# Optimization experiments

Hardware: AMD Instinct MI355X
Metric: run time of the kernel (lower is better)

The kernel has to match this reference:

```python
import jax, jax.numpy as jnp
import numpy as np

N_HEAD = 12
N_EMBD = 768


def setup_inputs() -> dict:
    key = jax.random.key(0)
    ks = jax.random.split(key, 5)
    B, T, C = 8, 1024, N_EMBD
    x = jax.random.normal(ks[0], (B, T, C), dtype=jnp.float32)
    # c_attn: Linear(C, 3C); c_proj: Linear(C, C). PyTorch Linear: y = x @ W.T + b
    s = 1.0 / np.sqrt(C)
    W_attn = jax.random.uniform(ks[1], (3 * C, C), minval=-s, maxval=s, dtype=jnp.float32)
    b_attn = jax.random.uniform(ks[2], (3 * C,), minval=-s, maxval=s, dtype=jnp.float32)
    W_proj = jax.random.uniform(ks[3], (C, C), minval=-s, maxval=s, dtype=jnp.float32)
    b_proj = jax.random.uniform(ks[4], (C,), minval=-s, maxval=s, dtype=jnp.float32)
    return {"x": x, "W_attn": W_attn, "b_attn": b_attn, "W_proj": W_proj, "b_proj": b_proj}


def reference(x, W_attn, b_attn, W_proj, b_proj):
    B, T, C = x.shape
    H = N_HEAD
    hs = C // H  # head size
    qkv = x @ W_attn.T + b_attn  # [B, T, 3C]
    q, k, v = jnp.split(qkv, 3, axis=2)
    # [B, T, H, hs] -> [B, H, T, hs]
    q = q.reshape(B, T, H, hs).transpose(0, 2, 1, 3)
    k = k.reshape(B, T, H, hs).transpose(0, 2, 1, 3)
    v = v.reshape(B, T, H, hs).transpose(0, 2, 1, 3)
    att = jnp.einsum('bhqd,bhkd->bhqk', q, k) * (1.0 / np.sqrt(hs))
    causal = jnp.tril(jnp.ones((T, T), dtype=bool))
    att = jnp.where(causal, att, -jnp.inf)
    att = jax.nn.softmax(att, axis=-1)
    y = jnp.einsum('bhqk,bhkd->bhqd', att, v)  # [B, H, T, hs]
    y = y.transpose(0, 2, 1, 3).reshape(B, T, C)
    return y @ W_proj.T + b_proj
```

## Files before the change

### kernel.cpp

```cpp
#include <hip/hip_runtime.h>

typedef unsigned short u16;
typedef __attribute__((ext_vector_type(8))) __bf16 bf16x8;
typedef __attribute__((ext_vector_type(4))) float f32x4;
typedef __attribute__((ext_vector_type(4))) int i32x4;

#define MFMA16(a, b, c) __builtin_amdgcn_mfma_f32_16x16x32_bf16(a, b, c, 0, 0, 0)

__device__ __forceinline__ u16 f2b(float f) {
  __bf16 h = (__bf16)f;
  return __builtin_bit_cast(u16, h);
}

__device__ __forceinline__ void gl_lds16(const void* g, void* l) {
  __builtin_amdgcn_global_load_lds(
      (const __attribute__((address_space(1))) void*)g,
      (__attribute__((address_space(3))) void*)l, 16, 0, 0);
}

__device__ __forceinline__ bf16x8 ldf(const void* p) {
  return __builtin_bit_cast(bf16x8, *(const i32x4*)p);
}

__global__ __launch_bounds__(256) void cvt3_kernel(
    const float4* __restrict__ a, ushort4* __restrict__ oa, int na4,
    const float4* __restrict__ b, ushort4* __restrict__ ob, int nb4,
    const float4* __restrict__ c, ushort4* __restrict__ oc, int nc4) {
  const int step = gridDim.x * blockDim.x;
  const int t0 = blockIdx.x * blockDim.x + threadIdx.x;
  for (int i = t0; i < na4; i += step) {
    float4 v = a[i];
    ushort4 o; o.x = f2b(v.x); o.y = f2b(v.y); o.z = f2b(v.z); o.w = f2b(v.w);
    oa[i] = o;
  }
  for (int i = t0; i < nb4; i += step) {
    float4 v = b[i];
    ushort4 o; o.x = f2b(v.x); o.y = f2b(v.y); o.z = f2b(v.z); o.w = f2b(v.w);
    ob[i] = o;
  }
  for (int i = t0; i < nc4; i += step) {
    float4 v = c[i];
    ushort4 o; o.x = f2b(v.x); o.y = f2b(v.y); o.z = f2b(v.z); o.w = f2b(v.w);
    oc[i] = o;
  }
}

template <int BM, int EPI>
__global__ __launch_bounds__(256, 3) void gemm4(
    const u16* __restrict__ A, const u16* __restrict__ B,
    const float* __restrict__ bias, int M, int N, int K,
    u16* __restrict__ q_s, u16* __restrict__ k_s, u16* __restrict__ vt_s,
    float* __restrict__ outf) {
  constexpr int BN = 192;
  constexpr int MR = BM / 32;
  constexpr int NR = 6;
  constexpr int IA = BM / 32;
  constexpr int IB = 6;
  __shared__ __align__(16) u16 As[BM * 64];
  __shared__ __align__(16) u16 Bs[BN * 64];
  const int tid = threadIdx.x;
  const int w = tid >> 6, l = tid & 63;
  const int lo = l & 15, hi = l >> 4;
  const int wr = w >> 1, wc = w & 1;
  const int nwg = gridDim.x * gridDim.y;
  int bid = blockIdx.y * gridDim.x + blockIdx.x;
  bid = (bid & 7) * (nwg >> 3) + (bid >> 3);
  const int bm0 = (bid / gridDim.x) * BM;
  const int bn0 = (bid % gridDim.x) * BN;
  const size_t Kb = (size_t)K * 2;
  const char* Ab = (const char*)A;
  const char* Bb = (const char*)B;
  const int lrow8 = l >> 3;
  const int lcol = (l & 7) * 16;

  f32x4 acc[MR][NR] = {};

  for (int kt = 0; kt < K; kt += 64) {
    __syncthreads();
#pragma unroll
    for (int i = 0; i < IA; ++i) {
      int rl = (w * IA + i) * 8 + lrow8;
      int cb = lcol ^ ((rl & 7) << 4);
      gl_lds16(Ab + (size_t)(bm0 + rl) * Kb + kt * 2 + cb,
               (char*)As + (w * IA + i) * 1024);
    }
#pragma unroll
    for (int i = 0; i < IB; ++i) {
      int rl = (w * IB + i) * 8 + lrow8;
      int cb = lcol ^ ((rl & 7) << 4);
      gl_lds16(Bb + (size_t)(bn0 + rl) * Kb + kt * 2 + cb,
               (char*)Bs + (w * IB + i) * 1024);
    }
    __syncthreads();
#pragma unroll
    for (int ks = 0; ks < 2; ++ks) {
      bf16x8 bfr[NR];
#pragma unroll
      for (int nf = 0; nf < NR; ++nf) {
        int r = wc * 96 + nf * 16 + lo;
        bfr[nf] = ldf((char*)Bs + r * 128 + ((ks * 64 + hi * 16) ^ ((r & 7) << 4)));
      }
#pragma unroll
      for (int mf = 0; mf < MR; ++mf) {
        int r = wr * (MR * 16) + mf * 16 + lo;
        bf16x8 afr = ldf((char*)As + r * 128 + ((ks * 64 + hi * 16) ^ ((r & 7) << 4)));
#pragma unroll
        for (int nf = 0; nf < NR; ++nf) acc[mf][nf] = MFMA16(afr, bfr[nf], acc[mf][nf]);
      }
    }
  }

#pragma unroll
  for (int nf = 0; nf < NR; ++nf) {
    int col = bn0 + wc * 96 + nf * 16 + lo;
    float bv = bias[col];
    if (EPI == 0) {
      int seg = col / 768;
      int cs = col - seg * 768;
      int h = cs >> 6, d = cs & 63;
      u16* dst = (seg == 0) ? q_s : k_s;
#pragma unroll
      for (int mf = 0; mf < MR; ++mf) {
        int m0 = bm0 + wr * (MR * 16) + mf * 16 + hi * 4;
        int bb = m0 >> 10, t0 = m0 & 1023;
        size_t bh = (size_t)(bb * 12 + h);
        if (seg < 2) {
#pragma unroll
          for (int r = 0; r < 4; ++r)
            dst[(bh * 1024 + t0 + r) * 64 + d] = f2b(acc[mf][nf][r] + bv);
        } else {
          ushort4 pk;
          pk.x = f2b(acc[mf][nf][0] + bv);
          pk.y = f2b(acc[mf][nf][1] + bv);
          pk.z = f2b(acc[mf][nf][2] + bv);
          pk.w = f2b(acc[mf][nf][3] + bv);
          *(ushort4*)&vt_s[(bh * 64 + d) * 1024 + t0] = pk;
        }
      }
    } else {
#pragma unroll
      for (int mf = 0; mf < MR; ++mf) {
        int m0 = bm0 + wr * (MR * 16) + mf * 16 + hi * 4;
#pragma unroll
        for (int r = 0; r < 4; ++r) outf[(size_t)(m0 + r) * N + col] = acc[mf][nf][r] + bv;
      }
    }
  }
}

__global__ __launch_bounds__(256) void attn_kernel(
    const u16* __restrict__ Q, const u16* __restrict__ Kg,
    const u16* __restrict__ Vt, u16* __restrict__ Y) {
  __shared__ __align__(16) u16 Ks[2][64 * 64];
  __shared__ __align__(16) u16 Vs[2][64 * 64];
  __shared__ __align__(16) u16 Ps[4][16 * 64];
  const int tid = threadIdx.x;
  const int w = tid >> 6, l = tid & 63;
  const int lo = l & 15, hi = l >> 4;
  int bid = blockIdx.y * gridDim.x + blockIdx.x;
  bid = (bid & 7) * 96 + (bid >> 3);
  const int bh = bid >> 3;
  const int pr = bid & 7;
  const int b = bh / 12, h = bh % 12;
  const float c1 = 0.125f * 1.44269504f;
  char* pw = (char*)&Ps[w][0];
  const int swl = (lo & 7) << 4;
  const u16* Qb = Q + (size_t)bh * 65536;
  const char* Kbp = (const char*)(Kg + (size_t)bh * 65536);
  const char* Vbp = (const char*)(Vt + (size_t)bh * 65536);

  bf16x8 onesv;
#pragma unroll
  for (int j = 0; j < 8; ++j) onesv[j] = (__bf16)1.0f;

  auto STAGE = [&](int buf, int kb) {
#pragma unroll
    for (int i = 0; i < 2; ++i) {
      int c = w * 2 + i;
      int row = c * 8 + (l >> 3);
      int cb = ((l & 7) * 16) ^ ((row & 7) << 4);
      gl_lds16(Kbp + (size_t)(kb + row) * 128 + cb, (char*)&Ks[buf][0] + c * 1024);
      gl_lds16(Vbp + (size_t)row * 2048 + (size_t)kb * 2 + cb, (char*)&Vs[buf][0] + c * 1024);
    }
  };

  for (int sg = 0; sg < 2; ++sg) {
    const int tile = sg ? (15 - pr) : pr;
    const int q0 = tile * 64 + w * 16;
    const int nt = tile + 1;

    bf16x8 qf[2];
#pragma unroll
    for (int ks = 0; ks < 2; ++ks)
      qf[ks] = ldf(Qb + (size_t)(q0 + lo) * 64 + ks * 32 + hi * 8);

    f32x4 o[4] = {};
    f32x4 mrow, lsum;
#pragma unroll
    for (int r = 0; r < 4; ++r) { mrow[r] = -1e30f; lsum[r] = 0.0f; }

    STAGE(0, 0);
    for (int kt = 0; kt < nt; ++kt) {
      const int cur = kt & 1;
      if (kt + 1 < nt) {
        STAGE(cur ^ 1, (kt + 1) * 64);
        asm volatile("s_waitcnt vmcnt(4)" ::: "memory");
      } else {
        asm volatile("s_waitcnt vmcnt(0)" ::: "memory");
      }
      __builtin_amdgcn_s_barrier();
      __builtin_amdgcn_sched_barrier(0);
      const char* Kt = (const char*)&Ks[cur][0];
      const char* Vv = (const char*)&Vs[cur][0];
      const int kb = kt * 64;

      f32x4 sv[4] = {};
      __builtin_amdgcn_s_setprio(1);
#pragma unroll
      for (int kf = 0; kf < 4; ++kf) {
        int rb = (kf * 16 + lo) * 128;
#pragma unroll
        for (int ks = 0; ks < 2; ++ks)
          sv[kf] = MFMA16(qf[ks], ldf(Kt + rb + ((ks * 64 + hi * 16) ^ swl)), sv[kf]);
      }
      __builtin_amdgcn_s_setprio(0);
      bf16x8 vb[4][2];
#pragma unroll
      for (int nd = 0; nd < 4; ++nd) {
        int rb = (nd * 16 + lo) * 128;
#pragma unroll
        for (int ks = 0; ks < 2; ++ks)
          vb[nd][ks] = ldf(Vv + rb + ((ks * 64 + hi * 16) ^ swl));
      }
      if (kt == nt - 1) {
#pragma unroll
        for (int kf = 0; kf < 4; ++kf)
#pragma unroll
          for (int r = 0; r < 4; ++r) {
            int qrow = q0 + hi * 4 + r;
            int kcol = kb + kf * 16 + lo;
            if (kcol > qrow) sv[kf][r] = -1e30f;
          }
      }
      f32x4 lm = sv[0];
#pragma unroll
      for (int kf = 1; kf < 4; ++kf)
#pragma unroll
        for (int r = 0; r < 4; ++r) lm[r] = fmaxf(lm[r], sv[kf][r]);
      bool need = false;
#pragma unroll
      for (int r = 0; r < 4; ++r) need |= (lm[r] * c1 > mrow[r] + 8.0f);
      if (__any(need)) {
#pragma unroll
        for (int st = 1; st < 16; st <<= 1)
#pragma unroll
          for (int r = 0; r < 4; ++r) lm[r] = fmaxf(lm[r], __shfl_xor(lm[r], st));
        f32x4 al;
#pragma unroll
        for (int r = 0; r < 4; ++r) {
          float Mn = fmaxf(mrow[r], lm[r] * c1);
          al[r] = __builtin_amdgcn_exp2f(mrow[r] - Mn);
          mrow[r] = Mn;
          lsum[r] *= al[r];
        }
#pragma unroll
        for (int nd = 0; nd < 4; ++nd)
#pragma unroll
          for (int r = 0; r < 4; ++r) o[nd][r] *= al[r];
      }
#pragma unroll
      for (int kf = 0; kf < 4; ++kf)
#pragma unroll
        for (int r = 0; r < 4; ++r)
          sv[kf][r] = __builtin_amdgcn_exp2f(fmaf(sv[kf][r], c1, -mrow[r]));
#pragma unroll
      for (int kf = 0; kf < 4; ++kf)
#pragma unroll
        for (int r = 0; r < 4; ++r) {
          int qrow = hi * 4 + r;
          int cb = ((lo + kf * 16) * 2) ^ ((qrow & 7) << 4);
          *(u16*)(pw + qrow * 128 + cb) = f2b(sv[kf][r]);
        }
      bf16x8 pa[2];
#pragma unroll
      for (int ks = 0; ks < 2; ++ks)
        pa[ks] = ldf(pw + lo * 128 + ((ks * 64 + hi * 16) ^ swl));
      __builtin_amdgcn_s_setprio(1);
#pragma unroll
      for (int ks = 0; ks < 2; ++ks) {
#pragma unroll
        for (int nd = 0; nd < 4; ++nd) o[nd] = MFMA16(pa[ks], vb[nd][ks], o[nd]);
        lsum = MFMA16(pa[ks], onesv, lsum);
      }
      __builtin_amdgcn_s_setprio(0);
      __builtin_amdgcn_sched_barrier(0);
      __builtin_amdgcn_s_barrier();
    }

    f32x4 inv;
#pragma unroll
    for (int r = 0; r < 4; ++r) inv[r] = 1.0f / lsum[r];
#pragma unroll
    for (int nd = 0; nd < 4; ++nd)
#pragma unroll
      for (int r = 0; r < 4; ++r) {
        int t = q0 + hi * 4 + r;
        int d = nd * 16 + lo;
        Y[((size_t)b * 1024 + t) * 768 + h * 64 + d] = f2b(o[nd][r] * inv[r]);
      }
  }
}

extern "C" void kernel_launch(void* const* d_in, const int* in_sizes, int n_in,
                              void* d_out, int out_size, void* d_ws, size_t ws_size,
                              hipStream_t stream) {
  const float* x  = (const float*)d_in[0];
  const float* Wa = (const float*)d_in[1];
  const float* ba = (const float*)d_in[2];
  const float* Wp = (const float*)d_in[3];
  const float* bp = (const float*)d_in[4];
  float* out = (float*)d_out;
  char* ws = (char*)d_ws;

  constexpr size_t XB  = 0;
  constexpr size_t WAB = 12582912;
  constexpr size_t WPB = WAB + 3538944;
  constexpr size_t QS  = WPB + 1179648;
  constexpr size_t KS  = QS + 12582912;
  constexpr size_t VTS = KS + 12582912;
  constexpr size_t YB  = VTS + 12582912;

  u16* xb  = (u16*)(ws + XB);
  u16* wab = (u16*)(ws + WAB);
  u16* wpb = (u16*)(ws + WPB);
  u16* qs  = (u16*)(ws + QS);
  u16* ks  = (u16*)(ws + KS);
  u16* vts = (u16*)(ws + VTS);
  u16* yb  = (u16*)(ws + YB);

  cvt3_kernel<<<2048, 256, 0, stream>>>(
      (const float4*)x,  (ushort4*)xb,  8192 * 768 / 4,
      (const float4*)Wa, (ushort4*)wab, 2304 * 768 / 4,
      (const float4*)Wp, (ushort4*)wpb, 768 * 768 / 4);

  gemm4<128, 0><<<dim3(12, 64), 256, 0, stream>>>(xb, wab, ba, 8192, 2304, 768,
                                                  qs, ks, vts, nullptr);
  attn_kernel<<<dim3(8, 96), 256, 0, stream>>>(qs, ks, vts, yb);
  gemm4<64, 1><<<dim3(4, 128), 256, 0, stream>>>(yb, wpb, bp, 8192, 768, 768,
                                                 nullptr, nullptr, nullptr, out);
}
```

Measured before the change: 99.84 us.

## Triple-buffer K/V staging and build P operand via shuffles instead of LDS

Moves K/V staging to a three-buffer ring with prefetch two tiles ahead, which removes the trailing barrier in each iteration. QK^T is computed transposed so each lane holds one query row. That lets the row max and rescale factor be computed per lane with fewer shuffles. The P matrix for the PV MFMA is now assembled with cross-lane shuffles rather than an LDS write/read round trip, at the cost of more shuffle instructions and more LDS for the extra K/V buffer.

New measurement: 113.8 us. +14.0%, slower.

```diff
diff --git a/kernel.cpp b/kernel.cpp
--- a/kernel.cpp
+++ b/kernel.cpp
@@ -1,6 +1,7 @@
 #include <hip/hip_runtime.h>
 
 typedef unsigned short u16;
+typedef unsigned int u32;
 typedef __attribute__((ext_vector_type(8))) __bf16 bf16x8;
 typedef __attribute__((ext_vector_type(4))) float f32x4;
 typedef __attribute__((ext_vector_type(4))) int i32x4;
@@ -151,9 +152,8 @@
 __global__ __launch_bounds__(256) void attn_kernel(
     const u16* __restrict__ Q, const u16* __restrict__ Kg,
     const u16* __restrict__ Vt, u16* __restrict__ Y) {
-  __shared__ __align__(16) u16 Ks[2][64 * 64];
-  __shared__ __align__(16) u16 Vs[2][64 * 64];
-  __shared__ __align__(16) u16 Ps[4][16 * 64];
+  __shared__ __align__(16) u16 Ks[3][64 * 64];
+  __shared__ __align__(16) u16 Vs[3][64 * 64];
   const int tid = threadIdx.x;
   const int w = tid >> 6, l = tid & 63;
   const int lo = l & 15, hi = l >> 4;
@@ -163,11 +163,12 @@
   const int pr = bid & 7;
   const int b = bh / 12, h = bh % 12;
   const float c1 = 0.125f * 1.44269504f;
-  char* pw = (char*)&Ps[w][0];
   const int swl = (lo & 7) << 4;
   const u16* Qb = Q + (size_t)bh * 65536;
   const char* Kbp = (const char*)(Kg + (size_t)bh * 65536);
   const char* Vbp = (const char*)(Vt + (size_t)bh * 65536);
+  const int shbase = lo + ((l & 16) ? 32 : 0);
+  const bool hiLow = (l & 32) == 0;
 
   bf16x8 onesv;
 #pragma unroll
@@ -188,6 +189,7 @@
     const int tile = sg ? (15 - pr) : pr;
     const int q0 = tile * 64 + w * 16;
     const int nt = tile + 1;
+    const int qr = q0 + lo;
 
     bf16x8 qf[2];
 #pragma unroll
@@ -195,33 +197,33 @@
       qf[ks] = ldf(Qb + (size_t)(q0 + lo) * 64 + ks * 32 + hi * 8);
 
     f32x4 o[4] = {};
-    f32x4 mrow, lsum;
-#pragma unroll
-    for (int r = 0; r < 4; ++r) { mrow[r] = -1e30f; lsum[r] = 0.0f; }
-
+    f32x4 lsum = {0.f, 0.f, 0.f, 0.f};
+    float mrow = -1e30f;
+
+    __builtin_amdgcn_s_barrier();
     STAGE(0, 0);
+    if (nt > 1) STAGE(1, 64);
+
     for (int kt = 0; kt < nt; ++kt) {
-      const int cur = kt & 1;
-      if (kt + 1 < nt) {
-        STAGE(cur ^ 1, (kt + 1) * 64);
+      if (kt + 1 < nt)
         asm volatile("s_waitcnt vmcnt(4)" ::: "memory");
-      } else {
+      else
         asm volatile("s_waitcnt vmcnt(0)" ::: "memory");
-      }
       __builtin_amdgcn_s_barrier();
       __builtin_amdgcn_sched_barrier(0);
-      const char* Kt = (const char*)&Ks[cur][0];
-      const char* Vv = (const char*)&Vs[cur][0];
+      if (kt + 2 < nt) STAGE((kt + 2) % 3, (kt + 2) * 64);
+      const char* Kt = (const char*)&Ks[kt % 3][0];
+      const char* Vv = (const char*)&Vs[kt % 3][0];
       const int kb = kt * 64;
 
-      f32x4 sv[4] = {};
+      f32x4 st[4] = {};
       __builtin_amdgcn_s_setprio(1);
 #pragma unroll
       for (int kf = 0; kf < 4; ++kf) {
         int rb = (kf * 16 + lo) * 128;
 #pragma unroll
         for (int ks = 0; ks < 2; ++ks)
-          sv[kf] = MFMA16(qf[ks], ldf(Kt + rb + ((ks * 64 + hi * 16) ^ swl)), sv[kf]);
+          st[kf] = MFMA16(ldf(Kt + rb + ((ks * 64 + hi * 16) ^ swl)), qf[ks], st[kf]);
       }
       __builtin_amdgcn_s_setprio(0);
       bf16x8 vb[4][2];
@@ -237,54 +239,55 @@
         for (int kf = 0; kf < 4; ++kf)
 #pragma unroll
           for (int r = 0; r < 4; ++r) {
-            int qrow = q0 + hi * 4 + r;
-            int kcol = kb + kf * 16 + lo;
-            if (kcol > qrow) sv[kf][r] = -1e30f;
+            int kcol = kb + kf * 16 + hi * 4 + r;
+            if (kcol > qr) st[kf][r] = -1e30f;
           }
       }
-      f32x4 lm = sv[0];
-#pragma unroll
-      for (int kf = 1; kf < 4; ++kf)
-#pragma unroll
-        for (int r = 0; r < 4; ++r) lm[r] = fmaxf(lm[r], sv[kf][r]);
-      bool need = false;
-#pragma unroll
-      for (int r = 0; r < 4; ++r) need |= (lm[r] * c1 > mrow[r] + 8.0f);
-      if (__any(need)) {
-#pragma unroll
-        for (int st = 1; st < 16; st <<= 1)
-#pragma unroll
-          for (int r = 0; r < 4; ++r) lm[r] = fmaxf(lm[r], __shfl_xor(lm[r], st));
-        f32x4 al;
-#pragma unroll
-        for (int r = 0; r < 4; ++r) {
-          float Mn = fmaxf(mrow[r], lm[r] * c1);
-          al[r] = __builtin_amdgcn_exp2f(mrow[r] - Mn);
-          mrow[r] = Mn;
-          lsum[r] *= al[r];
+      float lm = st[0][0];
+#pragma unroll
+      for (int kf = 0; kf < 4; ++kf)
+#pragma unroll
+        for (int r = 0; r < 4; ++r) lm = fmaxf(lm, st[kf][r]);
+      lm = fmaxf(lm, __shfl_xor(lm, 16));
+      lm = fmaxf(lm, __shfl_xor(lm, 32));
+      if (__any(lm * c1 > mrow + 8.0f)) {
+        float Mn = fmaxf(mrow, lm * c1);
+        float alP = __builtin_amdgcn_exp2f(mrow - Mn);
+        mrow = Mn;
+        f32x4 alo;
+#pragma unroll
+        for (int r = 0; r < 4; ++r) alo[r] = __shfl(alP, hi * 4 + r);
+#pragma unroll
+        for (int nd = 0; nd < 4; ++nd)
+#pragma unroll
+          for (int r = 0; r < 4; ++r) o[nd][r] *= alo[r];
+#pragma unroll
+        for (int r = 0; r < 4; ++r) lsum[r] *= alo[r];
+      }
+#pragma unroll
+      for (int kf = 0; kf < 4; ++kf)
+#pragma unroll
+        for (int r = 0; r < 4; ++r)
+          st[kf][r] = __builtin_amdgcn_exp2f(fmaf(st[kf][r], c1, -mrow));
+      u32 pk[4][2];
+#pragma unroll
+      for (int kf = 0; kf < 4; ++kf)
+#pragma unroll
+        for (int rp = 0; rp < 2; ++rp)
+          pk[kf][rp] = (u32)f2b(st[kf][2 * rp]) | ((u32)f2b(st[kf][2 * rp + 1]) << 16);
+      bf16x8 pa[2];
+#pragma unroll
+      for (int ks = 0; ks < 2; ++ks) {
+        i32x4 wv;
+#pragma unroll
+        for (int s = 0; s < 4; ++s) {
+          int src = shbase + ((s >> 1) << 4);
+          u32 xa = __shfl(pk[2 * ks][s & 1], src);
+          u32 xb = __shfl(pk[2 * ks + 1][s & 1], src);
+          wv[s] = (int)(hiLow ? xa : xb);
         }
-#pragma unroll
-        for (int nd = 0; nd < 4; ++nd)
-#pragma unroll
-          for (int r = 0; r < 4; ++r) o[nd][r] *= al[r];
-      }
-#pragma unroll
-      for (int kf = 0; kf < 4; ++kf)
-#pragma unroll
-        for (int r = 0; r < 4; ++r)
-          sv[kf][r] = __builtin_amdgcn_exp2f(fmaf(sv[kf][r], c1, -mrow[r]));
-#pragma unroll
-      for (int kf = 0; kf < 4; ++kf)
-#pragma unroll
-        for (int r = 0; r < 4; ++r) {
-          int qrow = hi * 4 + r;
-          int cb = ((lo + kf * 16) * 2) ^ ((qrow & 7) << 4);
-          *(u16*)(pw + qrow * 128 + cb) = f2b(sv[kf][r]);
-        }
-      bf16x8 pa[2];
-#pragma unroll
-      for (int ks = 0; ks < 2; ++ks)
-        pa[ks] = ldf(pw + lo * 128 + ((ks * 64 + hi * 16) ^ swl));
+        pa[ks] = __builtin_bit_cast(bf16x8, wv);
+      }
       __builtin_amdgcn_s_setprio(1);
 #pragma unroll
       for (int ks = 0; ks < 2; ++ks) {
@@ -293,8 +296,6 @@
         lsum = MFMA16(pa[ks], onesv, lsum);
       }
       __builtin_amdgcn_s_setprio(0);
-      __builtin_amdgcn_sched_barrier(0);
-      __builtin_amdgcn_s_barrier();
     }
 
     f32x4 inv;
```
